# Kernel tuning notes

Hardware: AMD Instinct MI355X
Metric: run time of the kernel (lower is better)

## Reference

```python
import jax, jax.numpy as jnp
import numpy as np

EMBED_DIM = 1024
N_HEADS = 16
HEAD_DIM = EMBED_DIM // N_HEADS


def setup_inputs() -> dict:
    key = jax.random.key(0)
    k_x, k_qw, k_qb, k_ow, k_ob = jax.random.split(key, 5)
    s = 1.0 / np.sqrt(EMBED_DIM)
    return {
        "x": jax.random.normal(k_x, (2, 2048, EMBED_DIM), dtype=jnp.float32),
        "qkv_w": jax.random.uniform(k_qw, (3 * EMBED_DIM, EMBED_DIM), jnp.float32, -s, s),
        "qkv_b": jax.random.uniform(k_qb, (3 * EMBED_DIM,), jnp.float32, -s, s),
        "out_w": jax.random.uniform(k_ow, (EMBED_DIM, EMBED_DIM), jnp.float32, -s, s),
        "out_b": jax.random.uniform(k_ob, (EMBED_DIM,), jnp.float32, -s, s),
    }


def reference(x, qkv_w, qkv_b, out_w, out_b):
    B, S, E = x.shape
    # fused QKV projection (torch Linear: x @ W^T + b)
    qkv = x @ qkv_w.T + qkv_b                      # [B,S,3E]
    qkv = qkv.reshape(B, S, N_HEADS, 3 * HEAD_DIM).transpose(0, 2, 1, 3)  # [B,H,S,3d]
    q, k, v = jnp.split(qkv, 3, axis=-1)           # each [B,H,S,d]
    scores = jnp.einsum("bhqd,bhkd->bhqk", q, k) / jnp.sqrt(jnp.float32(HEAD_DIM))
    weights = jax.nn.softmax(scores, axis=-1)      # [B,H,S,S]
    attn = jnp.einsum("bhqk,bhkd->bhqd", weights, v)
    attn = attn.transpose(0, 2, 1, 3).reshape(B, S, E)
    return attn @ out_w.T + out_b
```

## Files before the change

### kernel.cpp

```cpp
#include <hip/hip_runtime.h>
#include <hip/hip_bf16.h>


#define E_DIM   1024
#define NHEADS  16
#define HDIM    64
#define SEQ     2048
#define TOK     4096
#define QKV_DIM 3072
#define QK_STRIDE 2048
#define QSCALE_F 0.18033688011112042f

typedef __attribute__((ext_vector_type(8))) short bf16x8;
typedef __attribute__((ext_vector_type(4))) float f32x4;
typedef __attribute__((ext_vector_type(4))) int   i32x4;
typedef __attribute__((ext_vector_type(2))) int   i32x2;
typedef __attribute__((ext_vector_type(2))) __bf16 bf16x2_t;

#if __has_builtin(__builtin_amdgcn_exp2f)
#define EXP2F(x) __builtin_amdgcn_exp2f(x)
#else
#define EXP2F(x) exp2f(x)
#endif

__device__ __forceinline__ unsigned pack2bf(float a, float b) {
#if __has_builtin(__builtin_amdgcn_cvt_pk_bf16_f32)
    union { bf16x2_t v; unsigned u; } u;
    u.v = __builtin_amdgcn_cvt_pk_bf16_f32(a, b);
    return u.u;
#else
    union { float f; unsigned u; } ua, ub; ua.f = a; ub.f = b;
    unsigned ra = ua.u + 0x7FFF + ((ua.u >> 16) & 1);
    unsigned rb = ub.u + 0x7FFF + ((ub.u >> 16) & 1);
    return (ra >> 16) | (rb & 0xFFFF0000u);
#endif
}

__device__ __forceinline__ unsigned short f2bf(float x) {
    return (unsigned short)(pack2bf(x, x) & 0xFFFFu);
}

__device__ __forceinline__ void load_lds16(const void* g, void* l) {
    __builtin_amdgcn_global_load_lds(
        (const __attribute__((address_space(1))) void*)g,
        (__attribute__((address_space(3))) void*)l, 16, 0, 0);
}

__device__ __forceinline__ bf16x8 lds_read8(const unsigned short* p) {
    union { i32x4 i; bf16x8 b; } u;
    u.i = *(const i32x4*)p;
    return u.b;
}

__device__ __forceinline__ f32x4 mfma16(bf16x8 a, bf16x8 b, f32x4 c) {
    return __builtin_amdgcn_mfma_f32_16x16x32_bf16(a, b, c, 0, 0, 0);
}

__global__ void cast3_kernel(const float* __restrict__ a, unsigned short* __restrict__ oa, int na4,
                             const float* __restrict__ b, unsigned short* __restrict__ ob, int nb4,
                             const float* __restrict__ c, unsigned short* __restrict__ oc) {
    int i = blockIdx.x * blockDim.x + threadIdx.x;
    const float* src; unsigned short* dst; int j;
    if (i < na4)            { src = a; dst = oa; j = i; }
    else if (i < na4 + nb4) { src = b; dst = ob; j = i - na4; }
    else                    { src = c; dst = oc; j = i - na4 - nb4; }
    f32x4 v = ((const f32x4*)src)[j];
    union { i32x2 i2; unsigned u[2]; } o;
    o.u[0] = pack2bf(v.x, v.y);
    o.u[1] = pack2bf(v.z, v.w);
    ((i32x2*)dst)[j] = o.i2;
}

__global__ __launch_bounds__(256, 3)
void gemm_qkv_kernel(const unsigned short* __restrict__ A,
                     const unsigned short* __restrict__ B,
                     const float* __restrict__ bias,
                     unsigned short* __restrict__ qk,
                     unsigned short* __restrict__ vT,
                     int K) {
    __shared__ __align__(16) unsigned short As[128 * 64];
    __shared__ __align__(16) unsigned short Bs[128 * 64];

    const int tid  = threadIdx.x;
    const int wave = tid >> 6, lane = tid & 63;
    const int quad = lane >> 4, l16 = lane & 15;
    const int row0 = blockIdx.y * 128, col0 = blockIdx.x * 128;
    const int wr = (wave >> 1) * 64, wc = (wave & 1) * 64;

    f32x4 acc[4][4];
#pragma unroll
    for (int i = 0; i < 4; ++i)
#pragma unroll
        for (int j = 0; j < 4; ++j) acc[i][j] = (f32x4){0.f, 0.f, 0.f, 0.f};

    const int nkt = K >> 6;
    for (int kt = 0; kt < nkt; ++kt) {
        const int k0 = kt << 6;
#pragma unroll
        for (int i = 0; i < 4; ++i) {
            int p = i * 256 + tid;
            int r = p >> 3;
            int kc = (p & 7) ^ (r & 7);
            load_lds16(A + (size_t)(row0 + r) * K + k0 + kc * 8, &As[p * 8]);
        }
#pragma unroll
        for (int i = 0; i < 4; ++i) {
            int p = i * 256 + tid;
            int r = p >> 3;
            int kc = (p & 7) ^ (r & 7);
            load_lds16(B + (size_t)(col0 + r) * K + k0 + kc * 8, &Bs[p * 8]);
        }
        __syncthreads();

#pragma unroll
        for (int ks = 0; ks < 2; ++ks) {
            bf16x8 af[4], bfr[4];
#pragma unroll
            for (int rb = 0; rb < 4; ++rb) {
                int r_l  = wr + rb * 16 + l16;
                int phys = (ks * 4 + quad) ^ (l16 & 7);
                af[rb] = lds_read8(&As[r_l * 64 + phys * 8]);
            }
#pragma unroll
            for (int cb = 0; cb < 4; ++cb) {
                int r_l  = wc + cb * 16 + l16;
                int phys = (ks * 4 + quad) ^ (l16 & 7);
                bfr[cb] = lds_read8(&Bs[r_l * 64 + phys * 8]);
            }
#pragma unroll
            for (int rb = 0; rb < 4; ++rb)
#pragma unroll
                for (int cb = 0; cb < 4; ++cb)
                    acc[rb][cb] = mfma16(af[rb], bfr[cb], acc[rb][cb]);
        }
        __syncthreads();
    }

#pragma unroll
    for (int rb = 0; rb < 4; ++rb)
#pragma unroll
        for (int cb = 0; cb < 4; ++cb) {
            int col = col0 + wc + cb * 16 + l16;
            int h    = col / 192;
            int part = col - h * 192;
            float bv = bias[col];
            int row_b = row0 + wr + rb * 16 + quad * 4;
            float v[4];
#pragma unroll
            for (int reg = 0; reg < 4; ++reg) v[reg] = acc[rb][cb][reg] + bv;
            if (part < 128) {
                float sc = (part < 64) ? QSCALE_F : 1.0f;
                size_t base = (size_t)h * 128 + part;
#pragma unroll
                for (int reg = 0; reg < 4; ++reg)
                    qk[(size_t)(row_b + reg) * QK_STRIDE + base] = f2bf(v[reg] * sc);
            } else {
                int i  = part - 128;
                int b  = row_b >> 11;
                int s  = row_b & 2047;
                i32x2 pk;
                pk.x = (int)pack2bf(v[0], v[1]);
                pk.y = (int)pack2bf(v[2], v[3]);
                *(i32x2*)&vT[(((size_t)(b * 16 + h)) * 64 + i) * SEQ + s] = pk;
            }
        }
}

__global__ __launch_bounds__(256, 2)
void gemm2_kernel(const unsigned short* __restrict__ A,
                  const unsigned short* __restrict__ B,
                  const float* __restrict__ bias,
                  float* __restrict__ C, int M, int N, int K) {
    __shared__ __align__(16) unsigned short As[128 * 64];
    __shared__ __align__(16) unsigned short Bs[64 * 64];

    const int tid  = threadIdx.x;
    const int wave = tid >> 6, lane = tid & 63;
    const int quad = lane >> 4, l16 = lane & 15;
    const int row0 = blockIdx.y * 128, col0 = blockIdx.x * 64;
    const int wr = wave * 32;

    f32x4 acc[2][4];
#pragma unroll
    for (int i = 0; i < 2; ++i)
#pragma unroll
        for (int j = 0; j < 4; ++j) acc[i][j] = (f32x4){0.f, 0.f, 0.f, 0.f};

    const int nkt = K >> 6;
    for (int kt = 0; kt < nkt; ++kt) {
        const int k0 = kt << 6;
#pragma unroll
        for (int i = 0; i < 4; ++i) {
            int p = i * 256 + tid;
            int r = p >> 3;
            int kc = (p & 7) ^ (r & 7);
            load_lds16(A + (size_t)(row0 + r) * K + k0 + kc * 8, &As[p * 8]);
        }
#pragma unroll
        for (int i = 0; i < 2; ++i) {
            int p = i * 256 + tid;
            int r = p >> 3;
            int kc = (p & 7) ^ (r & 7);
            load_lds16(B + (size_t)(col0 + r) * K + k0 + kc * 8, &Bs[p * 8]);
        }
        __syncthreads();

#pragma unroll
        for (int ks = 0; ks < 2; ++ks) {
            bf16x8 af[2], bfr[4];
#pragma unroll
            for (int rb = 0; rb < 2; ++rb) {
                int r_l  = wr + rb * 16 + l16;
                int phys = (ks * 4 + quad) ^ (l16 & 7);
                af[rb] = lds_read8(&As[r_l * 64 + phys * 8]);
            }
#pragma unroll
            for (int cb = 0; cb < 4; ++cb) {
                int r_l  = cb * 16 + l16;
                int phys = (ks * 4 + quad) ^ (l16 & 7);
                bfr[cb] = lds_read8(&Bs[r_l * 64 + phys * 8]);
            }
#pragma unroll
            for (int rb = 0; rb < 2; ++rb)
#pragma unroll
                for (int cb = 0; cb < 4; ++cb)
                    acc[rb][cb] = mfma16(af[rb], bfr[cb], acc[rb][cb]);
        }
        __syncthreads();
    }

#pragma unroll
    for (int rb = 0; rb < 2; ++rb)
#pragma unroll
        for (int cb = 0; cb < 4; ++cb) {
            int col = col0 + cb * 16 + l16;
            float bv = bias[col];
#pragma unroll
            for (int reg = 0; reg < 4; ++reg) {
                int row = row0 + wr + rb * 16 + quad * 4 + reg;
                C[(size_t)row * N + col] = acc[rb][cb][reg] + bv;
            }
        }
}

__global__ __launch_bounds__(256, 4)
void attn_kernel(const unsigned short* __restrict__ qk,
                 const unsigned short* __restrict__ vT,
                 unsigned short* __restrict__ attn) {
    __shared__ __align__(16) unsigned short lds[20480];

    const int tid  = threadIdx.x;
    const int wave = tid >> 6, lane = tid & 63;
    const int quad = lane >> 4, l16 = lane & 15;
    const int bh = blockIdx.y;
    const int b = bh >> 4, h = bh & 15;
    const int q0 = blockIdx.x * 64;
    const size_t rowbase = (size_t)b * SEQ;
    const int qtok = q0 + wave * 16 + l16;
    const int sw3 = l16 & 7;

    const unsigned short* kroot = qk + rowbase * QK_STRIDE + h * 128 + 64;
    const unsigned short* vroot = vT + (size_t)bh * 64 * SEQ;

    int srow[2], scol[2];
#pragma unroll
    for (int i = 0; i < 2; ++i) {
        int p = i * 256 + tid;
        srow[i] = p >> 3;
        scol[i] = ((p & 7) ^ (srow[i] & 7)) * 8;
    }

    const int fO0 = l16 * 64 + ((quad ^ sw3) * 8);
    const int fO1 = l16 * 64 + (((4 + quad) ^ sw3) * 8);
    int pwO[4];
#pragma unroll
    for (int c4 = 0; c4 < 4; ++c4)
        pwO[c4] = 16384 + wave * 1024 + l16 * 64
                + (((c4 * 2 + (quad >> 1)) ^ sw3) * 8) + (quad & 1) * 4;
    const int prO0 = 16384 + wave * 1024 + fO0;
    const int prO1 = 16384 + wave * 1024 + fO1;

    union { short s[8]; bf16x8 v; } uon;
#pragma unroll
    for (int j = 0; j < 8; ++j) uon.s[j] = (short)0x3F80;
    const bf16x8 onesb = uon.v;

    bf16x8 qf[2];
#pragma unroll
    for (int ks = 0; ks < 2; ++ks) {
        const unsigned short* p =
            qk + (rowbase + qtok) * QK_STRIDE + h * 128 + ks * 32 + quad * 8;
        union { i32x4 i; bf16x8 b; } u;
        u.i = *(const i32x4*)p;
        qf[ks] = u.b;
    }

    f32x4 o[4];
#pragma unroll
    for (int ib = 0; ib < 4; ++ib) o[ib] = (f32x4){0.f, 0.f, 0.f, 0.f};
    f32x4 lacc = (f32x4){0.f, 0.f, 0.f, 0.f};

#pragma unroll
    for (int i = 0; i < 2; ++i) {
        int p = i * 256 + tid;
        load_lds16(kroot + srow[i] * QK_STRIDE + scol[i], &lds[p * 8]);
    }
#pragma unroll
    for (int i = 0; i < 2; ++i) {
        int p = i * 256 + tid;
        load_lds16(vroot + srow[i] * SEQ + scol[i], &lds[8192 + p * 8]);
    }

    for (int kt = 0; kt < SEQ / 64; ++kt) {
        const int cur = kt & 1;
        __syncthreads();

        if (kt < SEQ / 64 - 1) {
            const int kb = (kt + 1) * 64;
            const int nb = (cur ^ 1) * 4096;
#pragma unroll
            for (int i = 0; i < 2; ++i) {
                int p = i * 256 + tid;
                load_lds16(kroot + (size_t)(kb + srow[i]) * QK_STRIDE + scol[i],
                           &lds[nb + p * 8]);
            }
#pragma unroll
            for (int i = 0; i < 2; ++i) {
                int p = i * 256 + tid;
                load_lds16(vroot + srow[i] * SEQ + kb + scol[i],
                           &lds[8192 + nb + p * 8]);
            }
        }

        const unsigned short* ksb = &lds[cur * 4096];
        const unsigned short* vsb = &lds[8192 + cur * 4096];

        f32x4 s[4];
#pragma unroll
        for (int cb = 0; cb < 4; ++cb) s[cb] = (f32x4){0.f, 0.f, 0.f, 0.f};
#pragma unroll
        for (int cb = 0; cb < 4; ++cb) {
            bf16x8 kf = lds_read8(ksb + fO0 + cb * 1024);
            s[cb] = mfma16(kf, qf[0], s[cb]);
        }
#pragma unroll
        for (int cb = 0; cb < 4; ++cb) {
            bf16x8 kf = lds_read8(ksb + fO1 + cb * 1024);
            s[cb] = mfma16(kf, qf[1], s[cb]);
        }

#pragma unroll
        for (int c4 = 0; c4 < 4; ++c4) {
            i32x2 pk;
            pk.x = (int)pack2bf(EXP2F(s[c4][0]), EXP2F(s[c4][1]));
            pk.y = (int)pack2bf(EXP2F(s[c4][2]), EXP2F(s[c4][3]));
            *(i32x2*)&lds[pwO[c4]] = pk;
        }
        __asm__ volatile("s_waitcnt lgkmcnt(0)" ::: "memory");
        {
            bf16x8 pf0 = lds_read8(&lds[prO0]);
            lacc = mfma16(pf0, onesb, lacc);
#pragma unroll
            for (int ib = 0; ib < 4; ++ib) {
                bf16x8 vf = lds_read8(vsb + fO0 + ib * 1024);
                o[ib] = mfma16(pf0, vf, o[ib]);
            }
            bf16x8 pf1 = lds_read8(&lds[prO1]);
            lacc = mfma16(pf1, onesb, lacc);
#pragma unroll
            for (int ib = 0; ib < 4; ++ib) {
                bf16x8 vf = lds_read8(vsb + fO1 + ib * 1024);
                o[ib] = mfma16(pf1, vf, o[ib]);
            }
        }
    }

    float il[4];
#pragma unroll
    for (int r = 0; r < 4; ++r) il[r] = 1.0f / lacc[r];
#pragma unroll
    for (int ib = 0; ib < 4; ++ib)
#pragma unroll
        for (int r = 0; r < 4; ++r) {
            int t = q0 + wave * 16 + quad * 4 + r;
            attn[(rowbase + t) * E_DIM + h * 64 + ib * 16 + l16] =
                f2bf(o[ib][r] * il[r]);
        }
}

extern "C" void kernel_launch(void* const* d_in, const int* in_sizes, int n_in,
                              void* d_out, int out_size, void* d_ws, size_t ws_size,
                              hipStream_t stream) {
    const float* x     = (const float*)d_in[0];
    const float* qkv_w = (const float*)d_in[1];
    const float* qkv_b = (const float*)d_in[2];
    const float* out_w = (const float*)d_in[3];
    const float* out_b = (const float*)d_in[4];

    char* ws = (char*)d_ws;
    unsigned short* xb   = (unsigned short*)(ws);
    unsigned short* wqkv = (unsigned short*)(ws + 8388608);
    unsigned short* wout = (unsigned short*)(ws + 14680064);
    unsigned short* qk   = (unsigned short*)(ws + 16777216);
    unsigned short* attn = (unsigned short*)(ws + 33554432);
    unsigned short* vT   = (unsigned short*)(ws + 41943040);

    cast3_kernel<<<8192, 256, 0, stream>>>(x, xb, 1048576,
                                           qkv_w, wqkv, 786432,
                                           out_w, wout);

    gemm_qkv_kernel<<<dim3(24, 32), 256, 0, stream>>>(
        xb, wqkv, qkv_b, qk, vT, E_DIM);

    attn_kernel<<<dim3(32, 32), 256, 0, stream>>>(qk, vT, attn);

    gemm2_kernel<<<dim3(16, 32), 256, 0, stream>>>(
        attn, wout, out_b, (float*)d_out, TOK, E_DIM, E_DIM);
}
```

Measured before the change: 187.3 us.

## Process two 16-row query groups per wave in attention to reuse K/V fragments

Each attention block now covers 128 queries instead of 64, with every wave handling two 16-query groups. Each K and V fragment read from LDS feeds two MFMAs, which halves the K/V global-to-LDS traffic per query and the LDS reads per MFMA. In exchange, register use roughly doubles for accumulators, the launch bound drops to 2 blocks per CU, and the grid halves to 512 blocks, which may reduce occupancy and latency hiding.

```diff
diff --git a/kernel.cpp b/kernel.cpp
--- a/kernel.cpp
+++ b/kernel.cpp
@@ -243,20 +243,19 @@
         }
 }
 
-__global__ __launch_bounds__(256, 4)
+__global__ __launch_bounds__(256, 2)
 void attn_kernel(const unsigned short* __restrict__ qk,
                  const unsigned short* __restrict__ vT,
                  unsigned short* __restrict__ attn) {
-    __shared__ __align__(16) unsigned short lds[20480];
+    __shared__ __align__(16) unsigned short lds[24576];
 
     const int tid  = threadIdx.x;
     const int wave = tid >> 6, lane = tid & 63;
     const int quad = lane >> 4, l16 = lane & 15;
     const int bh = blockIdx.y;
     const int b = bh >> 4, h = bh & 15;
-    const int q0 = blockIdx.x * 64;
+    const int q0 = blockIdx.x * 128;
     const size_t rowbase = (size_t)b * SEQ;
-    const int qtok = q0 + wave * 16 + l16;
     const int sw3 = l16 & 7;
 
     const unsigned short* kroot = qk + rowbase * QK_STRIDE + h * 128 + 64;
@@ -272,33 +271,44 @@
 
     const int fO0 = l16 * 64 + ((quad ^ sw3) * 8);
     const int fO1 = l16 * 64 + (((4 + quad) ^ sw3) * 8);
-    int pwO[4];
-#pragma unroll
-    for (int c4 = 0; c4 < 4; ++c4)
-        pwO[c4] = 16384 + wave * 1024 + l16 * 64
-                + (((c4 * 2 + (quad >> 1)) ^ sw3) * 8) + (quad & 1) * 4;
-    const int prO0 = 16384 + wave * 1024 + fO0;
-    const int prO1 = 16384 + wave * 1024 + fO1;
+    int pwO[2][4], prO[2][2];
+#pragma unroll
+    for (int g = 0; g < 2; ++g) {
+        int base = 16384 + wave * 2048 + g * 1024;
+#pragma unroll
+        for (int c4 = 0; c4 < 4; ++c4)
+            pwO[g][c4] = base + l16 * 64
+                       + (((c4 * 2 + (quad >> 1)) ^ sw3) * 8) + (quad & 1) * 4;
+        prO[g][0] = base + fO0;
+        prO[g][1] = base + fO1;
+    }
 
     union { short s[8]; bf16x8 v; } uon;
 #pragma unroll
     for (int j = 0; j < 8; ++j) uon.s[j] = (short)0x3F80;
     const bf16x8 onesb = uon.v;
 
-    bf16x8 qf[2];
-#pragma unroll
-    for (int ks = 0; ks < 2; ++ks) {
-        const unsigned short* p =
-            qk + (rowbase + qtok) * QK_STRIDE + h * 128 + ks * 32 + quad * 8;
-        union { i32x4 i; bf16x8 b; } u;
-        u.i = *(const i32x4*)p;
-        qf[ks] = u.b;
-    }
-
-    f32x4 o[4];
-#pragma unroll
-    for (int ib = 0; ib < 4; ++ib) o[ib] = (f32x4){0.f, 0.f, 0.f, 0.f};
-    f32x4 lacc = (f32x4){0.f, 0.f, 0.f, 0.f};
+    bf16x8 qf[2][2];
+#pragma unroll
+    for (int g = 0; g < 2; ++g)
+#pragma unroll
+        for (int ks = 0; ks < 2; ++ks) {
+            const unsigned short* p =
+                qk + (rowbase + q0 + wave * 32 + g * 16 + l16) * QK_STRIDE
+                   + h * 128 + ks * 32 + quad * 8;
+            union { i32x4 i; bf16x8 b; } u;
+            u.i = *(const i32x4*)p;
+            qf[g][ks] = u.b;
+        }
+
+    f32x4 o[2][4];
+#pragma unroll
+    for (int g = 0; g < 2; ++g)
+#pragma unroll
+        for (int ib = 0; ib < 4; ++ib) o[g][ib] = (f32x4){0.f, 0.f, 0.f, 0.f};
+    f32x4 lacc[2];
+    lacc[0] = (f32x4){0.f, 0.f, 0.f, 0.f};
+    lacc[1] = (f32x4){0.f, 0.f, 0.f, 0.f};
 
 #pragma unroll
     for (int i = 0; i < 2; ++i) {
@@ -335,57 +345,72 @@
         const unsigned short* ksb = &lds[cur * 4096];
         const unsigned short* vsb = &lds[8192 + cur * 4096];
 
-        f32x4 s[4];
-#pragma unroll
-        for (int cb = 0; cb < 4; ++cb) s[cb] = (f32x4){0.f, 0.f, 0.f, 0.f};
+        f32x4 s[2][4];
+#pragma unroll
+        for (int g = 0; g < 2; ++g)
+#pragma unroll
+            for (int cb = 0; cb < 4; ++cb) s[g][cb] = (f32x4){0.f, 0.f, 0.f, 0.f};
 #pragma unroll
         for (int cb = 0; cb < 4; ++cb) {
             bf16x8 kf = lds_read8(ksb + fO0 + cb * 1024);
-            s[cb] = mfma16(kf, qf[0], s[cb]);
+            s[0][cb] = mfma16(kf, qf[0][0], s[0][cb]);
+            s[1][cb] = mfma16(kf, qf[1][0], s[1][cb]);
         }
 #pragma unroll
         for (int cb = 0; cb < 4; ++cb) {
             bf16x8 kf = lds_read8(ksb + fO1 + cb * 1024);
-            s[cb] = mfma16(kf, qf[1], s[cb]);
-        }
-
-#pragma unroll
-        for (int c4 = 0; c4 < 4; ++c4) {
-            i32x2 pk;
-            pk.x = (int)pack2bf(EXP2F(s[c4][0]), EXP2F(s[c4][1]));
-            pk.y = (int)pack2bf(EXP2F(s[c4][2]), EXP2F(s[c4][3]));
-            *(i32x2*)&lds[pwO[c4]] = pk;
-        }
+            s[0][cb] = mfma16(kf, qf[0][1], s[0][cb]);
+            s[1][cb] = mfma16(kf, qf[1][1], s[1][cb]);
+        }
+
+#pragma unroll
+        for (int g = 0; g < 2; ++g)
+#pragma unroll
+            for (int c4 = 0; c4 < 4; ++c4) {
+                i32x2 pk;
+                pk.x = (int)pack2bf(EXP2F(s[g][c4][0]), EXP2F(s[g][c4][1]));
+                pk.y = (int)pack2bf(EXP2F(s[g][c4][2]), EXP2F(s[g][c4][3]));
+                *(i32x2*)&lds[pwO[g][c4]] = pk;
+            }
         __asm__ volatile("s_waitcnt lgkmcnt(0)" ::: "memory");
         {
-            bf16x8 pf0 = lds_read8(&lds[prO0]);
-            lacc = mfma16(pf0, onesb, lacc);
+            bf16x8 pf[2][2];
+#pragma unroll
+            for (int g = 0; g < 2; ++g) {
+                pf[g][0] = lds_read8(&lds[prO[g][0]]);
+                pf[g][1] = lds_read8(&lds[prO[g][1]]);
+                lacc[g] = mfma16(pf[g][0], onesb, lacc[g]);
+                lacc[g] = mfma16(pf[g][1], onesb, lacc[g]);
+            }
 #pragma unroll
             for (int ib = 0; ib < 4; ++ib) {
                 bf16x8 vf = lds_read8(vsb + fO0 + ib * 1024);
-                o[ib] = mfma16(pf0, vf, o[ib]);
-            }
-            bf16x8 pf1 = lds_read8(&lds[prO1]);
-            lacc = mfma16(pf1, onesb, lacc);
+                o[0][ib] = mfma16(pf[0][0], vf, o[0][ib]);
+                o[1][ib] = mfma16(pf[1][0], vf, o[1][ib]);
+            }
 #pragma unroll
             for (int ib = 0; ib < 4; ++ib) {
                 bf16x8 vf = lds_read8(vsb + fO1 + ib * 1024);
-                o[ib] = mfma16(pf1, vf, o[ib]);
-            }
-        }
-    }
-
-    float il[4];
-#pragma unroll
-    for (int r = 0; r < 4; ++r) il[r] = 1.0f / lacc[r];
-#pragma unroll
-    for (int ib = 0; ib < 4; ++ib)
-#pragma unroll
-        for (int r = 0; r < 4; ++r) {
-            int t = q0 + wave * 16 + quad * 4 + r;
-            attn[(rowbase + t) * E_DIM + h * 64 + ib * 16 + l16] =
-                f2bf(o[ib][r] * il[r]);
-        }
+                o[0][ib] = mfma16(pf[0][1], vf, o[0][ib]);
+                o[1][ib] = mfma16(pf[1][1], vf, o[1][ib]);
+            }
+        }
+    }
+
+#pragma unroll
+    for (int g = 0; g < 2; ++g) {
+        float il[4];
+#pragma unroll
+        for (int r = 0; r < 4; ++r) il[r] = 1.0f / lacc[g][r];
+#pragma unroll
+        for (int ib = 0; ib < 4; ++ib)
+#pragma unroll
+            for (int r = 0; r < 4; ++r) {
+                int t = q0 + wave * 32 + g * 16 + quad * 4 + r;
+                attn[(rowbase + t) * E_DIM + h * 64 + ib * 16 + l16] =
+                    f2bf(o[g][ib][r] * il[r]);
+            }
+    }
 }
 
 extern "C" void kernel_launch(void* const* d_in, const int* in_sizes, int n_in,
@@ -412,7 +437,7 @@
     gemm_qkv_kernel<<<dim3(24, 32), 256, 0, stream>>>(
         xb, wqkv, qkv_b, qk, vT, E_DIM);
 
-    attn_kernel<<<dim3(32, 32), 256, 0, stream>>>(qk, vT, attn);
+    attn_kernel<<<dim3(16, 32), 256, 0, stream>>>(qk, vT, attn);
 
     gemm2_kernel<<<dim3(16, 32), 256, 0, stream>>>(
         attn, wout, out_b, (float*)d_out, TOK, E_DIM, E_DIM);
```

Result: no change. 190.8 us (+1.9%).
